# Kernel tuning notes

Hardware: AMD Instinct MI355X
Metric: run time of the kernel (lower is better)

## Reference

```python
import jax, jax.numpy as jnp
import numpy as np

SCALE_BASE = 512.0
GAMMA = 0.96875

def xpos(x, downscale=False):
    # x: (B, L, d). XPOS = rotary embedding with exponential position-dependent scale.
    B, L, d = x.shape
    half = d // 2
    scale_vec = (jnp.arange(0, d, 2, dtype=jnp.float32) + 0.4 * d) / (1.4 * d)  # (half,)
    pos = jnp.arange(L, dtype=jnp.float32)
    scale = scale_vec[None, :] ** (pos[:, None] / SCALE_BASE)  # (L, half)
    if downscale:
        scale = 1.0 / scale
    inv_freq = 1.0 / (10000.0 ** (jnp.arange(half, dtype=jnp.float32) / half))
    sinusoid = pos[:, None] * inv_freq[None, :]  # (L, half)
    sin_s = jnp.repeat(jnp.sin(sinusoid) * scale, 2, axis=-1)  # duplicate_interleave -> (L, d)
    cos_s = jnp.repeat(jnp.cos(sinusoid) * scale, 2, axis=-1)
    x1, x2 = x[..., ::2], x[..., 1::2]
    rot = jnp.stack((-x2, x1), axis=-1).reshape(x.shape)  # rotate_every_two
    return x * cos_s + rot * sin_s

def decay_mask(L, gamma):
    n = jnp.arange(L)[:, None]
    m = jnp.arange(L)[None, :]
    diff = n - m
    expo = jnp.where(diff >= 0, diff, 0).astype(jnp.float32)
    return jnp.where(diff >= 0, gamma ** expo, 0.0)  # (L, L) causal decay

def setup_inputs() -> dict:
    key = jax.random.key(0)
    kx, kq, kk, kv = jax.random.split(key, 4)
    B, L, H = 4, 2048, 1024
    hs = 1024  # head_size == v_dim
    X = jax.random.normal(kx, (B, L, H), dtype=jnp.float32)
    W_Q = jax.random.normal(kq, (H, hs), dtype=jnp.float32) / H
    W_K = jax.random.normal(kk, (H, hs), dtype=jnp.float32) / H
    W_V = jax.random.normal(kv, (H, hs), dtype=jnp.float32) / H
    return {"X": X, "W_Q": W_Q, "W_K": W_K, "W_V": W_V}

def reference(X, W_Q, W_K, W_V):
    L = X.shape[1]
    Q = xpos(X @ W_Q)
    K = xpos(X @ W_K, downscale=True)
    V = X @ W_V
    D = decay_mask(L, GAMMA)
    ret = jnp.einsum('bnd,bmd->bnm', Q, K) * D[None]  # (B, L, L)
    return ret @ V
```

## Files before the change

### kernel.cpp

```cpp
#include <hip/hip_runtime.h>
#include <cmath>

typedef __attribute__((ext_vector_type(8))) short short8;
typedef __attribute__((ext_vector_type(4))) short short4v;
typedef __attribute__((ext_vector_type(16))) float floatx16;
typedef unsigned short ushort_t;

#define LSEQ   2048
#define DMODEL 1024
#define BM 128
#define BN 128
#define BK 64
#define TPAD 136

#define L2GAMMA (-0.045803595f)
#define L2E4_512 (0.0259525632f)

__device__ __forceinline__ ushort_t f2b(float x) {
    union { float f; unsigned u; } v; v.f = x;
    unsigned r = v.u + 0x7fffu + ((v.u >> 16) & 1u);
    return (ushort_t)(r >> 16);
}

#define GLOAD_LDS16(gptr, lptr)                                                     \
    __builtin_amdgcn_global_load_lds(                                               \
        (const __attribute__((address_space(1))) unsigned int*)(gptr),              \
        (__attribute__((address_space(3))) unsigned int*)(lptr), 16, 0, 0)

__device__ __forceinline__ void gemm_core(
    const ushort_t* __restrict__ Ag, int lda, int aRow0,
    const ushort_t* __restrict__ Bg, int ldb, int bRow0,
    int kDepth, ushort_t* As, ushort_t* Bs, floatx16 acc[2][2])
{
    const int tid  = threadIdx.x;
    const int wave = tid >> 6, lane = tid & 63;
    const int wm = wave >> 1, wn = wave & 1;
    const int l31 = lane & 31, half = lane >> 5;
    const int srow = lane >> 3;
    const int scol = ((lane & 7) ^ srow) * 8;

    const ushort_t* ap[4];
    const ushort_t* bp[4];
    #pragma unroll
    for (int L = 0; L < 4; ++L) {
        int r = (wave * 4 + L) * 8 + srow;
        ap[L] = Ag + (size_t)(aRow0 + r) * lda + scol;
        bp[L] = Bg + (size_t)(bRow0 + r) * ldb + scol;
    }
    const int ldst = (lane >> 3) * BK + (lane & 7) * 8;

    for (int k0 = 0; k0 < kDepth; k0 += BK) {
        __syncthreads();
        #pragma unroll
        for (int L = 0; L < 4; ++L) {
            GLOAD_LDS16(ap[L], As + (wave * 4 + L) * (8 * BK) + ldst);
            GLOAD_LDS16(bp[L], Bs + (wave * 4 + L) * (8 * BK) + ldst);
            ap[L] += BK; bp[L] += BK;
        }
        __syncthreads();

        #pragma unroll
        for (int ks = 0; ks < 4; ++ks) {
            const int ch = ((ks * 2 + half) ^ (l31 & 7)) * 8;
            short8 a0 = *(const short8*)(As + (wm * 64      + l31) * BK + ch);
            short8 a1 = *(const short8*)(As + (wm * 64 + 32 + l31) * BK + ch);
            short8 b0 = *(const short8*)(Bs + (wn * 64      + l31) * BK + ch);
            short8 b1 = *(const short8*)(Bs + (wn * 64 + 32 + l31) * BK + ch);
            acc[0][0] = __builtin_amdgcn_mfma_f32_32x32x16_bf16(a0, b0, acc[0][0], 0, 0, 0);
            acc[0][1] = __builtin_amdgcn_mfma_f32_32x32x16_bf16(a0, b1, acc[0][1], 0, 0, 0);
            acc[1][0] = __builtin_amdgcn_mfma_f32_32x32x16_bf16(a1, b0, acc[1][0], 0, 0, 0);
            acc[1][1] = __builtin_amdgcn_mfma_f32_32x32x16_bf16(a1, b1, acc[1][1], 0, 0, 0);
        }
    }
}

__global__ __launch_bounds__(256) void xpos_table_kernel(float2* __restrict__ T)
{
    int idx = blockIdx.x * 256 + threadIdx.x;
    int l = idx & 2047;
    int p = (idx >> 11) & 511;
    int mode = idx >> 20;
    float sv = (2.0f * (float)p + 409.6f) * (1.0f / 1433.6f);
    float coeff = log2f(sv) * (1.0f / 512.0f) + L2GAMMA;
    float invf = exp2f(-(float)p * L2E4_512);
    float lf = (float)l;
    float s, c;
    sincosf(lf * invf, &s, &c);
    float g = exp2f((mode == 0 ? lf : -lf) * coeff);
    T[idx] = make_float2(c * g, s * g);
}

__global__ __launch_bounds__(256) void cast_x_kernel(
    const float4* __restrict__ X, short4v* __restrict__ Xb, int n4)
{
    int i = blockIdx.x * 256 + threadIdx.x;
    if (i < n4) {
        float4 v = X[i];
        short4v o;
        o.x = (short)f2b(v.x); o.y = (short)f2b(v.y);
        o.z = (short)f2b(v.z); o.w = (short)f2b(v.w);
        Xb[i] = o;
    }
}

__global__ __launch_bounds__(256) void wtrans_kernel(
    const float* __restrict__ Wq, const float* __restrict__ Wk,
    const float* __restrict__ Wv, ushort_t* __restrict__ Wt)
{
    const float* W = blockIdx.z == 0 ? Wq : blockIdx.z == 1 ? Wk : Wv;
    ushort_t* O = Wt + (size_t)blockIdx.z * (DMODEL * DMODEL);
    __shared__ float t[32][33];
    const int x = threadIdx.x & 31, y = (threadIdx.x >> 5) * 4;
    const int k0 = blockIdx.y * 32, n0 = blockIdx.x * 32;
    #pragma unroll
    for (int j = 0; j < 4; ++j)
        t[y + j][x] = W[(size_t)(k0 + y + j) * DMODEL + n0 + x];
    __syncthreads();
    #pragma unroll
    for (int j = 0; j < 4; ++j)
        O[(size_t)(n0 + y + j) * DMODEL + k0 + x] = f2b(t[x][y + j]);
}

__global__ __launch_bounds__(256, 4) void qkv_kernel(
    const ushort_t* __restrict__ Xb, const ushort_t* __restrict__ Wt,
    const float2* __restrict__ Tab,
    ushort_t* __restrict__ Q, ushort_t* __restrict__ Ko, ushort_t* __restrict__ Vt)
{
    __shared__ ushort_t smem[128 * TPAD];
    ushort_t* As = smem;
    ushort_t* Bs = smem + BM * BK;

    const int lin = blockIdx.x;
    const int inner = lin & 63;
    const int sup = lin >> 6;
    const int c = (sup % 3) * 8 + (inner & 7);
    const int r = (sup / 3) * 8 + (inner >> 3);
    const int mode = c >> 3;
    const int c0 = (c & 7) * BN;
    const int row0 = r * BM;

    floatx16 acc[2][2] = {};
    gemm_core(Xb, DMODEL, row0,
              Wt + (size_t)mode * (DMODEL * DMODEL), DMODEL, c0,
              DMODEL, As, Bs, acc);

    const int wave = threadIdx.x >> 6, lane = threadIdx.x & 63;
    const int wm = wave >> 1, wn = wave & 1;
    const int l31 = lane & 31, half = lane >> 5;
    const int rBase = row0 + wm * 64 + 4 * half;
    const int cBase = c0 + wn * 64 + l31;

    if (mode == 2) {
        const int colL0 = wn * 64 + l31;
        const int rowL0 = wm * 64 + 4 * half;
        __syncthreads();
        #pragma unroll
        for (int mi = 0; mi < 2; ++mi)
            #pragma unroll
            for (int ni = 0; ni < 2; ++ni)
                #pragma unroll
                for (int rg = 0; rg < 4; ++rg) {
                    short4v pk;
                    pk.x = (short)f2b(acc[mi][ni][rg * 4 + 0]);
                    pk.y = (short)f2b(acc[mi][ni][rg * 4 + 1]);
                    pk.z = (short)f2b(acc[mi][ni][rg * 4 + 2]);
                    pk.w = (short)f2b(acc[mi][ni][rg * 4 + 3]);
                    *(short4v*)(smem + (colL0 + ni * 32) * TPAD
                                     + rowL0 + mi * 32 + 8 * rg) = pk;
                }
        __syncthreads();
        const int t = threadIdx.x;
        const int colV = c0 + (t >> 1);
        const int lhalf = (t & 1) * 64;
        const int b = row0 >> 11, lpos0 = (row0 & 2047) + lhalf;
        #pragma unroll
        for (int i = 0; i < 8; ++i) {
            short8 vv = *(const short8*)(smem + (t >> 1) * TPAD + lhalf + i * 8);
            *(short8*)(Vt + (size_t)b * (LSEQ * DMODEL)
                          + (size_t)colV * LSEQ + lpos0 + i * 8) = vv;
        }
    } else {
        ushort_t* O = (mode == 0) ? Q : Ko;
        const float2* Tm = Tab + (size_t)mode * (512 * 2048);
        #pragma unroll
        for (int ni = 0; ni < 2; ++ni) {
            int col = cBase + ni * 32;
            const float2* tp = Tm + ((size_t)(col >> 1) << 11);
            #pragma unroll
            for (int mi = 0; mi < 2; ++mi)
                #pragma unroll
                for (int rg = 0; rg < 4; ++rg) {
                    int l0 = (rBase + mi * 32 + 8 * rg) & 2047;
                    float4 t01 = *(const float4*)(tp + l0);
                    float4 t23 = *(const float4*)(tp + l0 + 2);
                    float cs[8] = {t01.x, t01.y, t01.z, t01.w,
                                   t23.x, t23.y, t23.z, t23.w};
                    #pragma unroll
                    for (int q = 0; q < 4; ++q) {
                        int row = rBase + mi * 32 + 8 * rg + q;
                        float cc = cs[2 * q], ss = cs[2 * q + 1];
                        float v  = acc[mi][ni][rg * 4 + q];
                        float pv = __shfl_xor(v, 1);
                        float res = (lane & 1) ? fmaf(v, cc, pv * ss)
                                               : fmaf(v, cc, -pv * ss);
                        O[(size_t)row * DMODEL + col] = f2b(res);
                    }
                }
        }
    }
}

__global__ __launch_bounds__(256, 4) void score_kernel(
    const ushort_t* __restrict__ Q, const ushort_t* __restrict__ Kc,
    ushort_t* __restrict__ S)
{
    const int t = blockIdx.x, z = blockIdx.z;
    int bi, bj;
    if (t < 3) { bi = (t > 0); bj = t - (t > 0); }
    else { int u = t - 3; bi = 2 + u / 3; bj = bi - 2 + u % 3; }

    __shared__ ushort_t As[BM * BK], Bs[BN * BK];
    floatx16 acc[2][2] = {};
    const size_t zoff = (size_t)z * (LSEQ * DMODEL);
    gemm_core(Q + zoff, DMODEL, bi * BM, Kc + zoff, DMODEL, bj * BN,
              DMODEL, As, Bs, acc);

    const int wave = threadIdx.x >> 6, lane = threadIdx.x & 63;
    const int wm = wave >> 1, wn = wave & 1;
    const int l31 = lane & 31, half = lane >> 5;
    const int nBase = bi * BM + wm * 64 + 4 * half;
    const int mBase = bj * BN + wn * 64 + l31;
    ushort_t* Sz = S + (size_t)z * LSEQ * LSEQ;
    #pragma unroll
    for (int mi = 0; mi < 2; ++mi)
        #pragma unroll
        for (int ni = 0; ni < 2; ++ni) {
            int m = mBase + ni * 32;
            #pragma unroll
            for (int rg = 0; rg < 4; ++rg)
                #pragma unroll
                for (int q = 0; q < 4; ++q) {
                    int n = nBase + mi * 32 + 8 * rg + q;
                    Sz[(size_t)n * LSEQ + m] =
                        (m <= n) ? f2b(acc[mi][ni][rg * 4 + q]) : (ushort_t)0;
                }
        }
}

__global__ __launch_bounds__(256, 4) void av_kernel(
    const ushort_t* __restrict__ S, const ushort_t* __restrict__ Vt,
    float* __restrict__ Out)
{
    const int bx = blockIdx.x, bi = blockIdx.y, z = blockIdx.z;
    const int kLo = (bi >= 2) ? (bi - 2) * BM : 0;
    const int kW  = (bi + 1) * BM - kLo;
    __shared__ ushort_t As[BM * BK], Bs[BN * BK];
    floatx16 acc[2][2] = {};
    gemm_core(S + (size_t)z * LSEQ * LSEQ + kLo, LSEQ, bi * BM,
              Vt + (size_t)z * (LSEQ * DMODEL) + kLo, LSEQ, bx * BN,
              kW, As, Bs, acc);

    const int wave = threadIdx.x >> 6, lane = threadIdx.x & 63;
    const int wm = wave >> 1, wn = wave & 1;
    const int l31 = lane & 31, half = lane >> 5;
    const int rBase = bi * BM + wm * 64 + 4 * half;
    const int cBase = bx * BN + wn * 64 + l31;
    float* Oz = Out + (size_t)z * (LSEQ * DMODEL);
    #pragma unroll
    for (int mi = 0; mi < 2; ++mi)
        #pragma unroll
        for (int ni = 0; ni < 2; ++ni)
            #pragma unroll
            for (int rg = 0; rg < 4; ++rg)
                #pragma unroll
                for (int q = 0; q < 4; ++q)
                    Oz[(size_t)(rBase + mi * 32 + 8 * rg + q) * DMODEL
                       + cBase + ni * 32] = acc[mi][ni][rg * 4 + q];
}

extern "C" void kernel_launch(void* const* d_in, const int* in_sizes, int n_in,
                              void* d_out, int out_size, void* d_ws, size_t ws_size,
                              hipStream_t stream)
{
    const float* X  = (const float*)d_in[0];
    const float* Wq = (const float*)d_in[1];
    const float* Wk = (const float*)d_in[2];
    const float* Wv = (const float*)d_in[3];
    float* out = (float*)d_out;

    const size_t LH  = (size_t)LSEQ * DMODEL;
    const size_t WSZ = (size_t)DMODEL * DMODEL;
    const size_t SSZ = (size_t)LSEQ * LSEQ;
    const size_t TABN = (size_t)2 * 512 * 2048;

    size_t need4 = TABN * 8 + 2 * (3 * WSZ + 4 * (4 * LH + SSZ));
    const int bs = (ws_size >= need4) ? 4 : 1;

    float2* Tab = (float2*)d_ws;
    ushort_t* ws16 = (ushort_t*)(Tab + TABN);
    ushort_t* Wt = ws16;
    ushort_t* Xb = Wt + 3 * WSZ;
    ushort_t* Q  = Xb + (size_t)bs * LH;
    ushort_t* Kb = Q  + (size_t)bs * LH;
    ushort_t* Vt = Kb + (size_t)bs * LH;
    ushort_t* S  = Vt + (size_t)bs * LH;

    xpos_table_kernel<<<dim3(TABN / 256), 256, 0, stream>>>(Tab);
    wtrans_kernel<<<dim3(32, 32, 3), 256, 0, stream>>>(Wq, Wk, Wv, Wt);

    for (int p = 0; p < 4 / bs; ++p) {
        const float* Xp = X + (size_t)p * bs * LH;
        cast_x_kernel<<<dim3(bs * 2048), 256, 0, stream>>>(
            (const float4*)Xp, (short4v*)Xb, bs * (int)(LH / 4));
        qkv_kernel<<<dim3(24 * bs * 16), 256, 0, stream>>>(
            Xb, Wt, Tab, Q, Kb, Vt);
        score_kernel<<<dim3(45, 1, bs), 256, 0, stream>>>(Q, Kb, S);
        av_kernel<<<dim3(8, 16, bs), 256, 0, stream>>>(S, Vt,
            out + (size_t)p * bs * LH);
    }
}
```

Before: 226.9 us.

## Widen QKV projection tile to 128x256 with 512-thread blocks

```diff
diff --git a/kernel.cpp b/kernel.cpp
--- a/kernel.cpp
+++ b/kernel.cpp
@@ -11,6 +11,7 @@
 #define BM 128
 #define BN 128
 #define BK 64
+#define BN2 256
 #define TPAD 136
 
 #define L2GAMMA (-0.045803595f)
@@ -47,7 +48,7 @@
         ap[L] = Ag + (size_t)(aRow0 + r) * lda + scol;
         bp[L] = Bg + (size_t)(bRow0 + r) * ldb + scol;
     }
-    const int ldst = (lane >> 3) * BK + (lane & 7) * 8;
+    const int ldst = srow * BK + (lane & 7) * 8;
 
     for (int k0 = 0; k0 < kDepth; k0 += BK) {
         __syncthreads();
@@ -56,6 +57,57 @@
             GLOAD_LDS16(ap[L], As + (wave * 4 + L) * (8 * BK) + ldst);
             GLOAD_LDS16(bp[L], Bs + (wave * 4 + L) * (8 * BK) + ldst);
             ap[L] += BK; bp[L] += BK;
+        }
+        __syncthreads();
+
+        #pragma unroll
+        for (int ks = 0; ks < 4; ++ks) {
+            const int ch = ((ks * 2 + half) ^ (l31 & 7)) * 8;
+            short8 a0 = *(const short8*)(As + (wm * 64      + l31) * BK + ch);
+            short8 a1 = *(const short8*)(As + (wm * 64 + 32 + l31) * BK + ch);
+            short8 b0 = *(const short8*)(Bs + (wn * 64      + l31) * BK + ch);
+            short8 b1 = *(const short8*)(Bs + (wn * 64 + 32 + l31) * BK + ch);
+            acc[0][0] = __builtin_amdgcn_mfma_f32_32x32x16_bf16(a0, b0, acc[0][0], 0, 0, 0);
+            acc[0][1] = __builtin_amdgcn_mfma_f32_32x32x16_bf16(a0, b1, acc[0][1], 0, 0, 0);
+            acc[1][0] = __builtin_amdgcn_mfma_f32_32x32x16_bf16(a1, b0, acc[1][0], 0, 0, 0);
+            acc[1][1] = __builtin_amdgcn_mfma_f32_32x32x16_bf16(a1, b1, acc[1][1], 0, 0, 0);
+        }
+    }
+}
+
+__device__ __forceinline__ void gemm_core512(
+    const ushort_t* __restrict__ Ag, int lda, int aRow0,
+    const ushort_t* __restrict__ Bg, int ldb, int bRow0,
+    int kDepth, ushort_t* As, ushort_t* Bs, floatx16 acc[2][2])
+{
+    const int tid  = threadIdx.x;
+    const int w = tid >> 6, lane = tid & 63;
+    const int wm = w >> 2, wn = w & 3;
+    const int l31 = lane & 31, half = lane >> 5;
+    const int srow = lane >> 3;
+    const int scol = ((lane & 7) ^ srow) * 8;
+
+    const ushort_t* ap[2];
+    const ushort_t* bp[4];
+    #pragma unroll
+    for (int L = 0; L < 2; ++L)
+        ap[L] = Ag + (size_t)(aRow0 + (w + L * 8) * 8 + srow) * lda + scol;
+    #pragma unroll
+    for (int L = 0; L < 4; ++L)
+        bp[L] = Bg + (size_t)(bRow0 + (w + L * 8) * 8 + srow) * ldb + scol;
+    const int ldst = srow * BK + (lane & 7) * 8;
+
+    for (int k0 = 0; k0 < kDepth; k0 += BK) {
+        __syncthreads();
+        #pragma unroll
+        for (int L = 0; L < 2; ++L) {
+            GLOAD_LDS16(ap[L], As + (w + L * 8) * (8 * BK) + ldst);
+            ap[L] += BK;
+        }
+        #pragma unroll
+        for (int L = 0; L < 4; ++L) {
+            GLOAD_LDS16(bp[L], Bs + (w + L * 8) * (8 * BK) + ldst);
+            bp[L] += BK;
         }
         __syncthreads();
 
@@ -121,63 +173,64 @@
         O[(size_t)(n0 + y + j) * DMODEL + k0 + x] = f2b(t[x][y + j]);
 }
 
-__global__ __launch_bounds__(256, 4) void qkv_kernel(
+__global__ __launch_bounds__(512, 4) void qkv_kernel(
     const ushort_t* __restrict__ Xb, const ushort_t* __restrict__ Wt,
     const float2* __restrict__ Tab,
     ushort_t* __restrict__ Q, ushort_t* __restrict__ Ko, ushort_t* __restrict__ Vt)
 {
-    __shared__ ushort_t smem[128 * TPAD];
+    __shared__ ushort_t smem[(BM + BN2) * BK];
     ushort_t* As = smem;
     ushort_t* Bs = smem + BM * BK;
 
-    const int lin = blockIdx.x;
-    const int inner = lin & 63;
-    const int sup = lin >> 6;
-    const int c = (sup % 3) * 8 + (inner & 7);
-    const int r = (sup / 3) * 8 + (inner >> 3);
-    const int mode = c >> 3;
-    const int c0 = (c & 7) * BN;
-    const int row0 = r * BM;
+    const int ct = blockIdx.x;
+    const int mode = ct >> 2;
+    const int c0 = (ct & 3) * BN2;
+    const int row0 = blockIdx.y * BM;
 
     floatx16 acc[2][2] = {};
-    gemm_core(Xb, DMODEL, row0,
-              Wt + (size_t)mode * (DMODEL * DMODEL), DMODEL, c0,
-              DMODEL, As, Bs, acc);
-
-    const int wave = threadIdx.x >> 6, lane = threadIdx.x & 63;
-    const int wm = wave >> 1, wn = wave & 1;
+    gemm_core512(Xb, DMODEL, row0,
+                 Wt + (size_t)mode * (DMODEL * DMODEL), DMODEL, c0,
+                 DMODEL, As, Bs, acc);
+
+    const int w = threadIdx.x >> 6, lane = threadIdx.x & 63;
+    const int wm = w >> 2, wn = w & 3;
     const int l31 = lane & 31, half = lane >> 5;
     const int rBase = row0 + wm * 64 + 4 * half;
     const int cBase = c0 + wn * 64 + l31;
 
     if (mode == 2) {
-        const int colL0 = wn * 64 + l31;
-        const int rowL0 = wm * 64 + 4 * half;
-        __syncthreads();
-        #pragma unroll
-        for (int mi = 0; mi < 2; ++mi)
+        const int b = row0 >> 11, lpos0 = row0 & 2047;
+        const int t = threadIdx.x;
+        #pragma unroll
+        for (int h = 0; h < 2; ++h) {
+            __syncthreads();
+            if ((wn >> 1) == h) {
+                const int colL0 = (wn & 1) * 64 + l31;
+                #pragma unroll
+                for (int ni = 0; ni < 2; ++ni)
+                    #pragma unroll
+                    for (int mi = 0; mi < 2; ++mi)
+                        #pragma unroll
+                        for (int rg = 0; rg < 4; ++rg) {
+                            short4v pk;
+                            pk.x = (short)f2b(acc[mi][ni][rg * 4 + 0]);
+                            pk.y = (short)f2b(acc[mi][ni][rg * 4 + 1]);
+                            pk.z = (short)f2b(acc[mi][ni][rg * 4 + 2]);
+                            pk.w = (short)f2b(acc[mi][ni][rg * 4 + 3]);
+                            *(short4v*)(smem + (colL0 + ni * 32) * TPAD
+                                             + wm * 64 + 4 * half
+                                             + mi * 32 + 8 * rg) = pk;
+                        }
+            }
+            __syncthreads();
+            const int colV = c0 + h * 128 + (t >> 2);
+            const int r0 = (t & 3) * 32;
             #pragma unroll
-            for (int ni = 0; ni < 2; ++ni)
-                #pragma unroll
-                for (int rg = 0; rg < 4; ++rg) {
-                    short4v pk;
-                    pk.x = (short)f2b(acc[mi][ni][rg * 4 + 0]);
-                    pk.y = (short)f2b(acc[mi][ni][rg * 4 + 1]);
-                    pk.z = (short)f2b(acc[mi][ni][rg * 4 + 2]);
-                    pk.w = (short)f2b(acc[mi][ni][rg * 4 + 3]);
-                    *(short4v*)(smem + (colL0 + ni * 32) * TPAD
-                                     + rowL0 + mi * 32 + 8 * rg) = pk;
-                }
-        __syncthreads();
-        const int t = threadIdx.x;
-        const int colV = c0 + (t >> 1);
-        const int lhalf = (t & 1) * 64;
-        const int b = row0 >> 11, lpos0 = (row0 & 2047) + lhalf;
-        #pragma unroll
-        for (int i = 0; i < 8; ++i) {
-            short8 vv = *(const short8*)(smem + (t >> 1) * TPAD + lhalf + i * 8);
-            *(short8*)(Vt + (size_t)b * (LSEQ * DMODEL)
-                          + (size_t)colV * LSEQ + lpos0 + i * 8) = vv;
+            for (int i = 0; i < 4; ++i) {
+                short8 vv = *(const short8*)(smem + (t >> 2) * TPAD + r0 + i * 8);
+                *(short8*)(Vt + (size_t)b * (LSEQ * DMODEL)
+                              + (size_t)colV * LSEQ + lpos0 + r0 + i * 8) = vv;
+            }
         }
     } else {
         ushort_t* O = (mode == 0) ? Q : Ko;
@@ -312,7 +365,7 @@
         const float* Xp = X + (size_t)p * bs * LH;
         cast_x_kernel<<<dim3(bs * 2048), 256, 0, stream>>>(
             (const float4*)Xp, (short4v*)Xb, bs * (int)(LH / 4));
-        qkv_kernel<<<dim3(24 * bs * 16), 256, 0, stream>>>(
+        qkv_kernel<<<dim3(12, bs * 16), 512, 0, stream>>>(
             Xb, Wt, Tab, Q, Kb, Vt);
         score_kernel<<<dim3(45, 1, bs), 256, 0, stream>>>(Q, Kb, S);
         av_kernel<<<dim3(8, 16, bs), 256, 0, stream>>>(S, Vt,
```

New measurement: 227.5 us. No clear change (+0.2%).

## Double-buffer GEMM LDS tiles with BK=32 and drop grouped block swizzle in QKV

Applied to the files above, without the earlier changes.

```diff
diff --git a/kernel.cpp b/kernel.cpp
--- a/kernel.cpp
+++ b/kernel.cpp
@@ -10,7 +10,7 @@
 #define DMODEL 1024
 #define BM 128
 #define BN 128
-#define BK 64
+#define BK 32
 #define TPAD 136
 
 #define L2GAMMA (-0.045803595f)
@@ -27,50 +27,68 @@
         (const __attribute__((address_space(1))) unsigned int*)(gptr),              \
         (__attribute__((address_space(3))) unsigned int*)(lptr), 16, 0, 0)
 
+__device__ __forceinline__ void stage_tile(
+    const ushort_t* __restrict__ G, int ldg, int row0, int k,
+    ushort_t* Ls, int wave, int lane)
+{
+    const int rsub = lane >> 2;
+    const int gch  = ((lane & 3) ^ ((lane >> 3) & 3)) * 8;
+    #pragma unroll
+    for (int L = 0; L < 2; ++L) {
+        int j = wave * 2 + L;
+        GLOAD_LDS16(G + (size_t)(row0 + 16 * j + rsub) * ldg + k + gch,
+                    Ls + j * 512 + lane * 8);
+    }
+}
+
+__device__ __forceinline__ void mfma_slice(
+    const ushort_t* As, const ushort_t* Bs,
+    int wm, int wn, int l31, int half, floatx16 acc[2][2])
+{
+    const int sw = ((l31 >> 1) & 3);
+    #pragma unroll
+    for (int ks = 0; ks < 2; ++ks) {
+        const int cl = ks * 2 + half;
+        const int pos = (cl ^ sw) * 8;
+        short8 a0 = *(const short8*)(As + (wm * 64      + l31) * 32 + pos);
+        short8 a1 = *(const short8*)(As + (wm * 64 + 32 + l31) * 32 + pos);
+        short8 b0 = *(const short8*)(Bs + (wn * 64      + l31) * 32 + pos);
+        short8 b1 = *(const short8*)(Bs + (wn * 64 + 32 + l31) * 32 + pos);
+        acc[0][0] = __builtin_amdgcn_mfma_f32_32x32x16_bf16(a0, b0, acc[0][0], 0, 0, 0);
+        acc[0][1] = __builtin_amdgcn_mfma_f32_32x32x16_bf16(a0, b1, acc[0][1], 0, 0, 0);
+        acc[1][0] = __builtin_amdgcn_mfma_f32_32x32x16_bf16(a1, b0, acc[1][0], 0, 0, 0);
+        acc[1][1] = __builtin_amdgcn_mfma_f32_32x32x16_bf16(a1, b1, acc[1][1], 0, 0, 0);
+    }
+}
+
 __device__ __forceinline__ void gemm_core(
     const ushort_t* __restrict__ Ag, int lda, int aRow0,
     const ushort_t* __restrict__ Bg, int ldb, int bRow0,
-    int kDepth, ushort_t* As, ushort_t* Bs, floatx16 acc[2][2])
+    int kDepth, ushort_t* As0, ushort_t* Bs0, ushort_t* As1, ushort_t* Bs1,
+    floatx16 acc[2][2])
 {
     const int tid  = threadIdx.x;
     const int wave = tid >> 6, lane = tid & 63;
     const int wm = wave >> 1, wn = wave & 1;
     const int l31 = lane & 31, half = lane >> 5;
-    const int srow = lane >> 3;
-    const int scol = ((lane & 7) ^ srow) * 8;
-
-    const ushort_t* ap[4];
-    const ushort_t* bp[4];
-    #pragma unroll
-    for (int L = 0; L < 4; ++L) {
-        int r = (wave * 4 + L) * 8 + srow;
-        ap[L] = Ag + (size_t)(aRow0 + r) * lda + scol;
-        bp[L] = Bg + (size_t)(bRow0 + r) * ldb + scol;
-    }
-    const int ldst = (lane >> 3) * BK + (lane & 7) * 8;
-
-    for (int k0 = 0; k0 < kDepth; k0 += BK) {
+
+    stage_tile(Ag, lda, aRow0, 0, As0, wave, lane);
+    stage_tile(Bg, ldb, bRow0, 0, Bs0, wave, lane);
+
+    for (int k0 = 0; k0 < kDepth; k0 += 2 * BK) {
         __syncthreads();
-        #pragma unroll
-        for (int L = 0; L < 4; ++L) {
-            GLOAD_LDS16(ap[L], As + (wave * 4 + L) * (8 * BK) + ldst);
-            GLOAD_LDS16(bp[L], Bs + (wave * 4 + L) * (8 * BK) + ldst);
-            ap[L] += BK; bp[L] += BK;
-        }
+        if (k0 + BK < kDepth) {
+            stage_tile(Ag, lda, aRow0, k0 + BK, As1, wave, lane);
+            stage_tile(Bg, ldb, bRow0, k0 + BK, Bs1, wave, lane);
+        }
+        mfma_slice(As0, Bs0, wm, wn, l31, half, acc);
         __syncthreads();
-
-        #pragma unroll
-        for (int ks = 0; ks < 4; ++ks) {
-            const int ch = ((ks * 2 + half) ^ (l31 & 7)) * 8;
-            short8 a0 = *(const short8*)(As + (wm * 64      + l31) * BK + ch);
-            short8 a1 = *(const short8*)(As + (wm * 64 + 32 + l31) * BK + ch);
-            short8 b0 = *(const short8*)(Bs + (wn * 64      + l31) * BK + ch);
-            short8 b1 = *(const short8*)(Bs + (wn * 64 + 32 + l31) * BK + ch);
-            acc[0][0] = __builtin_amdgcn_mfma_f32_32x32x16_bf16(a0, b0, acc[0][0], 0, 0, 0);
-            acc[0][1] = __builtin_amdgcn_mfma_f32_32x32x16_bf16(a0, b1, acc[0][1], 0, 0, 0);
-            acc[1][0] = __builtin_amdgcn_mfma_f32_32x32x16_bf16(a1, b0, acc[1][0], 0, 0, 0);
-            acc[1][1] = __builtin_amdgcn_mfma_f32_32x32x16_bf16(a1, b1, acc[1][1], 0, 0, 0);
-        }
+        if (k0 + 2 * BK < kDepth) {
+            stage_tile(Ag, lda, aRow0, k0 + 2 * BK, As0, wave, lane);
+            stage_tile(Bg, ldb, bRow0, k0 + 2 * BK, Bs0, wave, lane);
+        }
+        if (k0 + BK < kDepth)
+            mfma_slice(As1, Bs1, wm, wn, l31, half, acc);
     }
 }
 
@@ -127,22 +145,19 @@
     ushort_t* __restrict__ Q, ushort_t* __restrict__ Ko, ushort_t* __restrict__ Vt)
 {
     __shared__ ushort_t smem[128 * TPAD];
-    ushort_t* As = smem;
-    ushort_t* Bs = smem + BM * BK;
-
-    const int lin = blockIdx.x;
-    const int inner = lin & 63;
-    const int sup = lin >> 6;
-    const int c = (sup % 3) * 8 + (inner & 7);
-    const int r = (sup / 3) * 8 + (inner >> 3);
-    const int mode = c >> 3;
-    const int c0 = (c & 7) * BN;
-    const int row0 = r * BM;
+    ushort_t* As0 = smem;
+    ushort_t* Bs0 = smem + 4096;
+    ushort_t* As1 = smem + 8192;
+    ushort_t* Bs1 = smem + 12288;
+
+    const int mode = blockIdx.x >> 3;
+    const int c0   = (blockIdx.x & 7) * BN;
+    const int row0 = blockIdx.y * BM;
 
     floatx16 acc[2][2] = {};
     gemm_core(Xb, DMODEL, row0,
               Wt + (size_t)mode * (DMODEL * DMODEL), DMODEL, c0,
-              DMODEL, As, Bs, acc);
+              DMODEL, As0, Bs0, As1, Bs1, acc);
 
     const int wave = threadIdx.x >> 6, lane = threadIdx.x & 63;
     const int wm = wave >> 1, wn = wave & 1;
@@ -219,11 +234,11 @@
     if (t < 3) { bi = (t > 0); bj = t - (t > 0); }
     else { int u = t - 3; bi = 2 + u / 3; bj = bi - 2 + u % 3; }
 
-    __shared__ ushort_t As[BM * BK], Bs[BN * BK];
+    __shared__ ushort_t smem[16384];
     floatx16 acc[2][2] = {};
     const size_t zoff = (size_t)z * (LSEQ * DMODEL);
     gemm_core(Q + zoff, DMODEL, bi * BM, Kc + zoff, DMODEL, bj * BN,
-              DMODEL, As, Bs, acc);
+              DMODEL, smem, smem + 4096, smem + 8192, smem + 12288, acc);
 
     const int wave = threadIdx.x >> 6, lane = threadIdx.x & 63;
     const int wm = wave >> 1, wn = wave & 1;
@@ -254,11 +269,11 @@
     const int bx = blockIdx.x, bi = blockIdx.y, z = blockIdx.z;
     const int kLo = (bi >= 2) ? (bi - 2) * BM : 0;
     const int kW  = (bi + 1) * BM - kLo;
-    __shared__ ushort_t As[BM * BK], Bs[BN * BK];
+    __shared__ ushort_t smem[16384];
     floatx16 acc[2][2] = {};
     gemm_core(S + (size_t)z * LSEQ * LSEQ + kLo, LSEQ, bi * BM,
               Vt + (size_t)z * (LSEQ * DMODEL) + kLo, LSEQ, bx * BN,
-              kW, As, Bs, acc);
+              kW, smem, smem + 4096, smem + 8192, smem + 12288, acc);
 
     const int wave = threadIdx.x >> 6, lane = threadIdx.x & 63;
     const int wm = wave >> 1, wn = wave & 1;
@@ -312,7 +327,7 @@
         const float* Xp = X + (size_t)p * bs * LH;
         cast_x_kernel<<<dim3(bs * 2048), 256, 0, stream>>>(
             (const float4*)Xp, (short4v*)Xb, bs * (int)(LH / 4));
-        qkv_kernel<<<dim3(24 * bs * 16), 256, 0, stream>>>(
+        qkv_kernel<<<dim3(24, bs * 16), 256, 0, stream>>>(
             Xb, Wt, Tab, Q, Kb, Vt);
         score_kernel<<<dim3(45, 1, bs), 256, 0, stream>>>(Q, Kb, S);
         av_kernel<<<dim3(8, 16, bs), 256, 0, stream>>>(S, Vt,
```

Result: no change. 230.5 us (+1.6%).
